# Optimization experiments

Measured on AMD Instinct MI355X. Metric: run time of the kernel, lower is better.

The kernel has to match this reference:

```python
import jax, jax.numpy as jnp
import numpy as np

B, W, H, C = 4, 32, 32, 128   # image feature map
S, D = 256, 512               # text seq len, text embed dim
NC = 64                       # num_channels (attention inner dim)


def setup_inputs() -> dict:
    key = jax.random.key(0)
    ks = jax.random.split(key, 16)
    def dense(k, din, dout):
        return jax.random.normal(k, (din, dout), jnp.float32) / np.sqrt(din)
    return {
        "x": jax.random.normal(ks[0], (B, W, H, C), jnp.float32),
        "s": jax.random.normal(ks[1], (B, S, D), jnp.float32),
        "a": jax.random.randint(ks[2], (B, S), 0, 2).astype(jnp.float32),
        "Wq": dense(ks[3], C, NC),  "bq": jnp.zeros((NC,), jnp.float32),
        "Wkx": dense(ks[4], C, NC), "bkx": jnp.zeros((NC,), jnp.float32),
        "Wvx": dense(ks[5], C, NC), "bvx": jnp.zeros((NC,), jnp.float32),
        "Wks": dense(ks[6], D, NC), "bks": jnp.zeros((NC,), jnp.float32),
        "Wvs": dense(ks[7], D, NC), "bvs": jnp.zeros((NC,), jnp.float32),
        "Wout": dense(ks[8], NC, C), "bout": jnp.zeros((C,), jnp.float32),
        "ln_scale": jnp.ones((C,), jnp.float32),
        "ln_bias": jnp.zeros((C,), jnp.float32),
    }


def reference(x, s, a, Wq, bq, Wkx, bkx, Wvx, bvx, Wks, bks, Wvs, bvs,
              Wout, bout, ln_scale, ln_bias):
    nc = Wq.shape[-1]
    # mask text embeddings: repeat(a,'b s -> b s d') * s
    te = s * a[:, :, None]
    # projections
    q = x @ Wq + bq            # (b,w,h,c)
    kx = x @ Wkx + bkx         # (b,w,h,c)
    vx = x @ Vx_dummy if False else x @ Wvx + bvx
    ks = te @ Wks + bks        # (b,s,c)
    vs = te @ Wvs + bvs        # (b,s,c)
    # broadcast-add spatial and text keys/values -> (b,w,h,s,c)
    k = kx[:, :, :, None, :] + ks[:, None, None, :, :]
    v = vx[:, :, :, None, :] + vs[:, None, None, :, :]
    # attention matrix over channels: v^T @ k contracted over s -> (b,w,h,c,c)
    attn = jnp.einsum('bwhsc,bwhsd->bwhcd', v, k) / jnp.sqrt(jnp.asarray(nc, x.dtype))
    attn = jax.nn.softmax(attn, axis=-1)
    # q applied through the channel-channel attention -> (b,w,h,c)
    out = jnp.einsum('bwhj,bwhjk->bwhk', q, attn)
    # output projection back to x channels, residual, layernorm
    out = out @ Wout + bout
    x = x + out
    mu = jnp.mean(x, axis=-1, keepdims=True)
    var = jnp.var(x, axis=-1, keepdims=True)
    x = (x - mu) * jax.lax.rsqrt(var + 1e-6) * ln_scale + ln_bias
    return x
```

## Files before the change

kernel.cpp:

```cpp
#include <hip/hip_runtime.h>
#include <hip/hip_bf16.h>

#define BB 4
#define SS 256
#define DD 512
#define CC 128
#define NC 64
#define PXB 8

__global__ __launch_bounds__(256) void text_proj_kernel(
    const float* __restrict__ s, const float* __restrict__ a,
    const float* __restrict__ Wks, const float* __restrict__ bks,
    const float* __restrict__ Wvs, const float* __restrict__ bvs,
    float* __restrict__ ksw, float* __restrict__ vsw)
{
    __shared__ float tel[4][DD];
    __shared__ float part[2][2][4][NC];
    const int t = threadIdx.x;
    const int w = t >> 6;
    const int lane = t & 63;
    const int row0 = blockIdx.x * 4;

    {
        const float4* s4 = (const float4*)(s + (size_t)row0 * DD);
        for (int i = t; i < 512; i += 256) {
            const int r = i >> 7;
            const float am = a[row0 + r];
            float4 v = s4[i];
            v.x *= am; v.y *= am; v.z *= am; v.w *= am;
            ((float4*)&tel[0][0])[i] = v;
        }
    }
    __syncthreads();

    const int m = w & 1;
    const int h = w >> 1;
    const float* __restrict__ Wm = m ? Wvs : Wks;
    const int kb = h * 256;
    float a0 = 0.f, a1 = 0.f, a2 = 0.f, a3 = 0.f;
    #pragma unroll 4
    for (int k = 0; k < 256; ++k) {
        const float wv = Wm[(size_t)(kb + k) * NC + lane];
        a0 = fmaf(tel[0][kb + k], wv, a0);
        a1 = fmaf(tel[1][kb + k], wv, a1);
        a2 = fmaf(tel[2][kb + k], wv, a2);
        a3 = fmaf(tel[3][kb + k], wv, a3);
    }
    part[m][h][0][lane] = a0; part[m][h][1][lane] = a1;
    part[m][h][2][lane] = a2; part[m][h][3][lane] = a3;
    __syncthreads();

    for (int i = t; i < 512; i += 256) {
        const int mm = i >> 8;
        const int r = (i >> 6) & 3;
        const int col = i & 63;
        const float v = part[mm][0][r][col] + part[mm][1][r][col]
                      + (mm ? bvs[col] : bks[col]);
        float* dst = mm ? vsw : ksw;
        dst[(size_t)(row0 + r) * NC + col] = v;
    }
}

__global__ __launch_bounds__(256) void reduce_kernel(
    const float* __restrict__ ksw, const float* __restrict__ vsw,
    float* __restrict__ Mw, float* __restrict__ Ksw, float* __restrict__ Vsw)
{
    __shared__ float pm[4][NC], pk[4][NC], pv[4];
    const int t = threadIdx.x, w = t >> 6, d = t & 63;
    const int b = blockIdx.x >> 6, c = blockIdx.x & 63;
    const float* __restrict__ vsb = vsw + (size_t)b * SS * NC;
    const float* __restrict__ ksb = ksw + (size_t)b * SS * NC;
    float acc = 0.f, ks_ = 0.f, vs_ = 0.f;
    #pragma unroll 4
    for (int j = 0; j < 64; ++j) {
        const int s2 = w * 64 + j;
        const float vv = vsb[s2 * NC + c];
        const float kv = ksb[s2 * NC + d];
        acc = fmaf(vv, kv, acc);
        ks_ += kv; vs_ += vv;
    }
    pm[w][d] = acc; pk[w][d] = ks_;
    if (d == 0) pv[w] = vs_;
    __syncthreads();
    if (t < 64) {
        Mw[((size_t)b * NC + c) * NC + t] = pm[0][t] + pm[1][t] + pm[2][t] + pm[3][t];
        if (c == 0) Ksw[b * NC + t] = pk[0][t] + pk[1][t] + pk[2][t] + pk[3][t];
        if (t == 0) Vsw[b * NC + c] = pv[0] + pv[1] + pv[2] + pv[3];
    }
}

__global__ __launch_bounds__(512) void pixel_kernel(
    const float* __restrict__ x,
    const float* __restrict__ Wq,  const float* __restrict__ bq,
    const float* __restrict__ Wkx, const float* __restrict__ bkx,
    const float* __restrict__ Wvx, const float* __restrict__ bvx,
    const float* __restrict__ Wout, const float* __restrict__ bout,
    const float* __restrict__ ln_scale, const float* __restrict__ ln_bias,
    const float* __restrict__ Mw, const float* __restrict__ Ksw,
    const float* __restrict__ Vsw,
    float* __restrict__ out)
{
    __shared__ float Wc[32 * 192];
    __shared__ float xl[PXB][CC];
    __shared__ float Ml[NC * 65];
    __shared__ float proj[3][PXB][NC];
    __shared__ float rsl[PXB][NC];
    __shared__ float mxl[PXB][NC];
    __shared__ float outl[PXB][NC];
    __shared__ float Ksl[NC], Vsl[NC];
    __shared__ float redl[4][2][4];

    const int t = threadIdx.x;
    const int w = t >> 6, lane = t & 63;
    const int px0g = blockIdx.x * PXB;
    const int b = px0g >> 10;

    {
        const float4* x4 = (const float4*)(x + (size_t)px0g * CC);
        for (int i = t; i < PXB * CC / 4; i += 512)
            ((float4*)&xl[0][0])[i] = x4[i];
        const float* Mb = Mw + (size_t)b * NC * NC;
        for (int i = t; i < NC * NC; i += 512)
            Ml[(i >> 6) * 65 + (i & 63)] = Mb[i];
        if (t < NC) { Ksl[t] = Ksw[b * NC + t]; Vsl[t] = Vsw[b * NC + t]; }
    }

    float4 pre0, pre1, pre2;
    {
        #pragma unroll
        for (int i = 0; i < 3; ++i) {
            const int flat = (t + i * 512) * 4;
            const int kk2 = flat / 192, col = flat % 192;
            const int seg = col >> 6, c0 = col & 63;
            const float* p = (seg == 0) ? Wq : (seg == 1 ? Wkx : Wvx);
            const float4 v = *(const float4*)(p + (size_t)kk2 * NC + c0);
            if (i == 0) pre0 = v; else if (i == 1) pre1 = v; else pre2 = v;
        }
    }
    const int mm = w % 3;
    const int g  = w / 3;
    float acc0 = 0.f, acc1 = 0.f, acc2 = 0.f, acc3 = 0.f;
    for (int kc = 0; kc < 4; ++kc) {
        ((float4*)Wc)[t]        = pre0;
        ((float4*)Wc)[t + 512]  = pre1;
        ((float4*)Wc)[t + 1024] = pre2;
        __syncthreads();
        if (kc < 3) {
            #pragma unroll
            for (int i = 0; i < 3; ++i) {
                const int flat = (t + i * 512) * 4;
                const int kk2 = flat / 192, col = flat % 192;
                const int seg = col >> 6, c0 = col & 63;
                const float* p = (seg == 0) ? Wq : (seg == 1 ? Wkx : Wvx);
                const float4 v = *(const float4*)(p + (size_t)((kc + 1) * 32 + kk2) * NC + c0);
                if (i == 0) pre0 = v; else if (i == 1) pre1 = v; else pre2 = v;
            }
        }
        if (w < 6) {
            const int kb = kc * 32;
            #pragma unroll
            for (int k4 = 0; k4 < 8; ++k4) {
                const float4 x0 = *(const float4*)&xl[4 * g + 0][kb + k4 * 4];
                const float4 x1 = *(const float4*)&xl[4 * g + 1][kb + k4 * 4];
                const float4 x2 = *(const float4*)&xl[4 * g + 2][kb + k4 * 4];
                const float4 x3 = *(const float4*)&xl[4 * g + 3][kb + k4 * 4];
                #pragma unroll
                for (int q = 0; q < 4; ++q) {
                    const float wv = Wc[(k4 * 4 + q) * 192 + mm * 64 + lane];
                    const float e0 = (q == 0) ? x0.x : (q == 1) ? x0.y : (q == 2) ? x0.z : x0.w;
                    const float e1 = (q == 0) ? x1.x : (q == 1) ? x1.y : (q == 2) ? x1.z : x1.w;
                    const float e2 = (q == 0) ? x2.x : (q == 1) ? x2.y : (q == 2) ? x2.z : x2.w;
                    const float e3 = (q == 0) ? x3.x : (q == 1) ? x3.y : (q == 2) ? x3.z : x3.w;
                    acc0 = fmaf(e0, wv, acc0);
                    acc1 = fmaf(e1, wv, acc1);
                    acc2 = fmaf(e2, wv, acc2);
                    acc3 = fmaf(e3, wv, acc3);
                }
            }
        }
        __syncthreads();
    }
    if (w < 6) {
        const float* bias = (mm == 0) ? bq : (mm == 1 ? bkx : bvx);
        const float bb = bias[lane];
        proj[mm][4 * g + 0][lane] = acc0 + bb;
        proj[mm][4 * g + 1][lane] = acc1 + bb;
        proj[mm][4 * g + 2][lane] = acc2 + bb;
        proj[mm][4 * g + 3][lane] = acc3 + bb;
    }
    __syncthreads();

    {
        const int px = w, c = lane;
        const float vxc = proj[2][px][c];
        const float qc  = proj[0][px][c];
        const float uc  = fmaf(256.0f, vxc, Vsl[c]);
        float row[NC];
        float mx = -3.4e38f;
        #pragma unroll
        for (int d = 0; d < NC; ++d) {
            const float A = fmaf(uc, proj[1][px][d],
                                 fmaf(vxc, Ksl[d], Ml[c * 65 + d])) * 0.125f;
            row[d] = A;
            mx = fmaxf(mx, A);
        }
        float sum = 0.f;
        #pragma unroll
        for (int d = 0; d < NC; ++d) sum += __expf(row[d] - mx);
        rsl[px][c] = qc / sum;
        mxl[px][c] = mx;
    }
    __syncthreads();

    {
        const int px = w, d = lane;
        const float kxd = proj[1][px][d];
        const float Ksd = Ksl[d];
        float acc = 0.f;
        #pragma unroll 4
        for (int c = 0; c < NC; ++c) {
            const float vxc = proj[2][px][c];
            const float uc = fmaf(256.0f, vxc, Vsl[c]);
            const float A = fmaf(uc, kxd, fmaf(vxc, Ksd, Ml[c * 65 + d])) * 0.125f;
            acc = fmaf(rsl[px][c], __expf(A - mxl[px][c]), acc);
        }
        outl[px][d] = acc;
    }
    __syncthreads();

    {
        const int col = t & 127;
        const int pxg = t >> 7;
        const int px0 = 2 * pxg, px1 = px0 + 1;
        float acc0 = 0.f, acc1 = 0.f;
        #pragma unroll 4
        for (int k = 0; k < NC; ++k) {
            const float wv = Wout[k * CC + col];
            acc0 = fmaf(outl[px0][k], wv, acc0);
            acc1 = fmaf(outl[px1][k], wv, acc1);
        }
        const float bb = bout[col];
        const float y0 = acc0 + bb + xl[px0][col];
        const float y1 = acc1 + bb + xl[px1][col];

        float s10 = y0, s20 = y0 * y0, s11 = y1, s21 = y1 * y1;
        #pragma unroll
        for (int off = 32; off >= 1; off >>= 1) {
            s10 += __shfl_down(s10, off);
            s20 += __shfl_down(s20, off);
            s11 += __shfl_down(s11, off);
            s21 += __shfl_down(s21, off);
        }
        const int half = (t >> 6) & 1;
        if (lane == 0) {
            redl[pxg][half][0] = s10; redl[pxg][half][1] = s20;
            redl[pxg][half][2] = s11; redl[pxg][half][3] = s21;
        }
        __syncthreads();
        const float S10 = redl[pxg][0][0] + redl[pxg][1][0];
        const float S20 = redl[pxg][0][1] + redl[pxg][1][1];
        const float S11 = redl[pxg][0][2] + redl[pxg][1][2];
        const float S21 = redl[pxg][0][3] + redl[pxg][1][3];
        const float mu0 = S10 * (1.f / 128.f);
        const float var0 = S20 * (1.f / 128.f) - mu0 * mu0;
        const float mu1 = S11 * (1.f / 128.f);
        const float var1 = S21 * (1.f / 128.f) - mu1 * mu1;
        const float r0 = rsqrtf(var0 + 1e-6f), r1 = rsqrtf(var1 + 1e-6f);
        const float gg = ln_scale[col], be = ln_bias[col];
        out[(size_t)(px0g + px0) * CC + col] = (y0 - mu0) * r0 * gg + be;
        out[(size_t)(px0g + px1) * CC + col] = (y1 - mu1) * r1 * gg + be;
    }
}

extern "C" void kernel_launch(void* const* d_in, const int* in_sizes, int n_in,
                              void* d_out, int out_size, void* d_ws, size_t ws_size,
                              hipStream_t stream) {
    const float* x        = (const float*)d_in[0];
    const float* s        = (const float*)d_in[1];
    const float* a        = (const float*)d_in[2];
    const float* Wq       = (const float*)d_in[3];
    const float* bq       = (const float*)d_in[4];
    const float* Wkx      = (const float*)d_in[5];
    const float* bkx      = (const float*)d_in[6];
    const float* Wvx      = (const float*)d_in[7];
    const float* bvx      = (const float*)d_in[8];
    const float* Wks      = (const float*)d_in[9];
    const float* bks      = (const float*)d_in[10];
    const float* Wvs      = (const float*)d_in[11];
    const float* bvs      = (const float*)d_in[12];
    const float* Wout     = (const float*)d_in[13];
    const float* bout     = (const float*)d_in[14];
    const float* ln_scale = (const float*)d_in[15];
    const float* ln_bias  = (const float*)d_in[16];

    float* ws  = (float*)d_ws;
    float* ksw = ws;
    float* vsw = ws + 65536;
    float* Mw  = ws + 131072;
    float* Ksw = ws + 147456;
    float* Vsw = ws + 147712;

    text_proj_kernel<<<(BB * SS) / 4, 256, 0, stream>>>(s, a, Wks, bks, Wvs, bvs, ksw, vsw);
    reduce_kernel<<<BB * NC, 256, 0, stream>>>(ksw, vsw, Mw, Ksw, Vsw);
    pixel_kernel<<<(BB * 1024) / PXB, 512, 0, stream>>>(
        x, Wq, bq, Wkx, bkx, Wvx, bvx, Wout, bout, ln_scale, ln_bias,
        Mw, Ksw, Vsw, (float*)d_out);
}
```

Before: 136.0 us.

## Split pixel projections into separate kernel and shrink per-block pixel tiles

Moves the q/kx/vx projections of x out of the pixel kernel into a standalone xproj kernel that writes a 192-wide projection buffer to workspace. The pixel kernel then loads these projections instead of staging weight chunks through shared memory, and drops to 4 pixels per block with 256 threads, doubling the block count. The text projection kernel is also reworked to handle 2 rows per block, with float4 weight loads and shuffle reductions across k-subgroups. This trades an extra launch and a global round-trip for the projections against higher occupancy and less synchronisation in the pixel kernel.

```diff
diff --git a/kernel.cpp b/kernel.cpp
--- a/kernel.cpp
+++ b/kernel.cpp
@@ -6,7 +6,49 @@
 #define DD 512
 #define CC 128
 #define NC 64
-#define PXB 8
+#define PXB 4
+
+__global__ __launch_bounds__(192) void xproj_kernel(
+    const float* __restrict__ x,
+    const float* __restrict__ Wq,  const float* __restrict__ bq,
+    const float* __restrict__ Wkx, const float* __restrict__ bkx,
+    const float* __restrict__ Wvx, const float* __restrict__ bvx,
+    float* __restrict__ P)
+{
+    __shared__ float xl[8][CC];
+    const int t = threadIdx.x;
+    const int w = t >> 6, lane = t & 63;
+    const int px0 = blockIdx.x * 8;
+
+    {
+        const float4* x4 = (const float4*)(x + (size_t)px0 * CC);
+        for (int i = t; i < 8 * CC / 4; i += 192)
+            ((float4*)&xl[0][0])[i] = x4[i];
+    }
+    __syncthreads();
+
+    const float* __restrict__ Wm = (w == 0) ? Wq : (w == 1 ? Wkx : Wvx);
+    const float* __restrict__ bm = (w == 0) ? bq : (w == 1 ? bkx : bvx);
+    float a0=0.f,a1=0.f,a2=0.f,a3=0.f,a4=0.f,a5=0.f,a6=0.f,a7=0.f;
+    #pragma unroll 4
+    for (int k = 0; k < CC; ++k) {
+        const float wv = Wm[(size_t)k * NC + lane];
+        a0 = fmaf(xl[0][k], wv, a0);
+        a1 = fmaf(xl[1][k], wv, a1);
+        a2 = fmaf(xl[2][k], wv, a2);
+        a3 = fmaf(xl[3][k], wv, a3);
+        a4 = fmaf(xl[4][k], wv, a4);
+        a5 = fmaf(xl[5][k], wv, a5);
+        a6 = fmaf(xl[6][k], wv, a6);
+        a7 = fmaf(xl[7][k], wv, a7);
+    }
+    const float bb = bm[lane];
+    float* dst = P + (size_t)px0 * 192 + w * 64 + lane;
+    dst[0*192] = a0 + bb; dst[1*192] = a1 + bb;
+    dst[2*192] = a2 + bb; dst[3*192] = a3 + bb;
+    dst[4*192] = a4 + bb; dst[5*192] = a5 + bb;
+    dst[6*192] = a6 + bb; dst[7*192] = a7 + bb;
+}
 
 __global__ __launch_bounds__(256) void text_proj_kernel(
     const float* __restrict__ s, const float* __restrict__ a,
@@ -14,46 +56,56 @@
     const float* __restrict__ Wvs, const float* __restrict__ bvs,
     float* __restrict__ ksw, float* __restrict__ vsw)
 {
-    __shared__ float tel[4][DD];
-    __shared__ float part[2][2][4][NC];
+    __shared__ float tel[2][DD];
+    __shared__ float part[2][2][2][NC];
     const int t = threadIdx.x;
-    const int w = t >> 6;
-    const int lane = t & 63;
-    const int row0 = blockIdx.x * 4;
+    const int w = t >> 6, lane = t & 63;
+    const int row0 = blockIdx.x * 2;
 
     {
         const float4* s4 = (const float4*)(s + (size_t)row0 * DD);
-        for (int i = t; i < 512; i += 256) {
-            const int r = i >> 7;
-            const float am = a[row0 + r];
-            float4 v = s4[i];
-            v.x *= am; v.y *= am; v.z *= am; v.w *= am;
-            ((float4*)&tel[0][0])[i] = v;
-        }
-    }
-    __syncthreads();
-
-    const int m = w & 1;
-    const int h = w >> 1;
+        const int i = t;
+        const int r = i >> 7;
+        const float am = a[row0 + r];
+        float4 v = s4[i];
+        v.x *= am; v.y *= am; v.z *= am; v.w *= am;
+        ((float4*)&tel[0][0])[i] = v;
+    }
+    __syncthreads();
+
+    const int m = w & 1, h = w >> 1;
+    const int kb = h * 256;
+    const int cg = (lane & 15) * 4;
+    const int ksub = lane >> 4;
     const float* __restrict__ Wm = m ? Wvs : Wks;
-    const int kb = h * 256;
-    float a0 = 0.f, a1 = 0.f, a2 = 0.f, a3 = 0.f;
+
+    float4 acc0 = {0,0,0,0}, acc1 = {0,0,0,0};
     #pragma unroll 4
-    for (int k = 0; k < 256; ++k) {
-        const float wv = Wm[(size_t)(kb + k) * NC + lane];
-        a0 = fmaf(tel[0][kb + k], wv, a0);
-        a1 = fmaf(tel[1][kb + k], wv, a1);
-        a2 = fmaf(tel[2][kb + k], wv, a2);
-        a3 = fmaf(tel[3][kb + k], wv, a3);
-    }
-    part[m][h][0][lane] = a0; part[m][h][1][lane] = a1;
-    part[m][h][2][lane] = a2; part[m][h][3][lane] = a3;
-    __syncthreads();
-
-    for (int i = t; i < 512; i += 256) {
-        const int mm = i >> 8;
-        const int r = (i >> 6) & 3;
-        const int col = i & 63;
+    for (int j = 0; j < 64; ++j) {
+        const int k = kb + 4 * j + ksub;
+        const float4 wv = *(const float4*)(Wm + (size_t)k * NC + cg);
+        const float t0 = tel[0][k];
+        const float t1 = tel[1][k];
+        acc0.x = fmaf(t0, wv.x, acc0.x); acc0.y = fmaf(t0, wv.y, acc0.y);
+        acc0.z = fmaf(t0, wv.z, acc0.z); acc0.w = fmaf(t0, wv.w, acc0.w);
+        acc1.x = fmaf(t1, wv.x, acc1.x); acc1.y = fmaf(t1, wv.y, acc1.y);
+        acc1.z = fmaf(t1, wv.z, acc1.z); acc1.w = fmaf(t1, wv.w, acc1.w);
+    }
+    #pragma unroll
+    for (int off = 16; off <= 32; off <<= 1) {
+        acc0.x += __shfl_down(acc0.x, off); acc0.y += __shfl_down(acc0.y, off);
+        acc0.z += __shfl_down(acc0.z, off); acc0.w += __shfl_down(acc0.w, off);
+        acc1.x += __shfl_down(acc1.x, off); acc1.y += __shfl_down(acc1.y, off);
+        acc1.z += __shfl_down(acc1.z, off); acc1.w += __shfl_down(acc1.w, off);
+    }
+    if (lane < 16) {
+        *(float4*)&part[m][h][0][cg] = acc0;
+        *(float4*)&part[m][h][1][cg] = acc1;
+    }
+    __syncthreads();
+
+    {
+        const int mm = t >> 7, r = (t >> 6) & 1, col = t & 63;
         const float v = part[mm][0][r][col] + part[mm][1][r][col]
                       + (mm ? bvs[col] : bks[col]);
         float* dst = mm ? vsw : ksw;
@@ -89,26 +141,22 @@
     }
 }
 
-__global__ __launch_bounds__(512) void pixel_kernel(
-    const float* __restrict__ x,
-    const float* __restrict__ Wq,  const float* __restrict__ bq,
-    const float* __restrict__ Wkx, const float* __restrict__ bkx,
-    const float* __restrict__ Wvx, const float* __restrict__ bvx,
+__global__ __launch_bounds__(256) void pixel_kernel(
+    const float* __restrict__ x, const float* __restrict__ P,
     const float* __restrict__ Wout, const float* __restrict__ bout,
     const float* __restrict__ ln_scale, const float* __restrict__ ln_bias,
     const float* __restrict__ Mw, const float* __restrict__ Ksw,
     const float* __restrict__ Vsw,
     float* __restrict__ out)
 {
-    __shared__ float Wc[32 * 192];
+    __shared__ float Ml[NC * 65];
+    __shared__ float projl[PXB][192];
     __shared__ float xl[PXB][CC];
-    __shared__ float Ml[NC * 65];
-    __shared__ float proj[3][PXB][NC];
     __shared__ float rsl[PXB][NC];
     __shared__ float mxl[PXB][NC];
     __shared__ float outl[PXB][NC];
     __shared__ float Ksl[NC], Vsl[NC];
-    __shared__ float redl[4][2][4];
+    __shared__ float redl[2][2][4];
 
     const int t = threadIdx.x;
     const int w = t >> 6, lane = t & 63;
@@ -116,90 +164,29 @@
     const int b = px0g >> 10;
 
     {
+        const float4* P4 = (const float4*)(P + (size_t)px0g * 192);
+        for (int i = t; i < PXB * 192 / 4; i += 256)
+            ((float4*)&projl[0][0])[i] = P4[i];
         const float4* x4 = (const float4*)(x + (size_t)px0g * CC);
-        for (int i = t; i < PXB * CC / 4; i += 512)
+        for (int i = t; i < PXB * CC / 4; i += 256)
             ((float4*)&xl[0][0])[i] = x4[i];
         const float* Mb = Mw + (size_t)b * NC * NC;
-        for (int i = t; i < NC * NC; i += 512)
+        for (int i = t; i < NC * NC; i += 256)
             Ml[(i >> 6) * 65 + (i & 63)] = Mb[i];
         if (t < NC) { Ksl[t] = Ksw[b * NC + t]; Vsl[t] = Vsw[b * NC + t]; }
     }
-
-    float4 pre0, pre1, pre2;
-    {
-        #pragma unroll
-        for (int i = 0; i < 3; ++i) {
-            const int flat = (t + i * 512) * 4;
-            const int kk2 = flat / 192, col = flat % 192;
-            const int seg = col >> 6, c0 = col & 63;
-            const float* p = (seg == 0) ? Wq : (seg == 1 ? Wkx : Wvx);
-            const float4 v = *(const float4*)(p + (size_t)kk2 * NC + c0);
-            if (i == 0) pre0 = v; else if (i == 1) pre1 = v; else pre2 = v;
-        }
-    }
-    const int mm = w % 3;
-    const int g  = w / 3;
-    float acc0 = 0.f, acc1 = 0.f, acc2 = 0.f, acc3 = 0.f;
-    for (int kc = 0; kc < 4; ++kc) {
-        ((float4*)Wc)[t]        = pre0;
-        ((float4*)Wc)[t + 512]  = pre1;
-        ((float4*)Wc)[t + 1024] = pre2;
-        __syncthreads();
-        if (kc < 3) {
-            #pragma unroll
-            for (int i = 0; i < 3; ++i) {
-                const int flat = (t + i * 512) * 4;
-                const int kk2 = flat / 192, col = flat % 192;
-                const int seg = col >> 6, c0 = col & 63;
-                const float* p = (seg == 0) ? Wq : (seg == 1 ? Wkx : Wvx);
-                const float4 v = *(const float4*)(p + (size_t)((kc + 1) * 32 + kk2) * NC + c0);
-                if (i == 0) pre0 = v; else if (i == 1) pre1 = v; else pre2 = v;
-            }
-        }
-        if (w < 6) {
-            const int kb = kc * 32;
-            #pragma unroll
-            for (int k4 = 0; k4 < 8; ++k4) {
-                const float4 x0 = *(const float4*)&xl[4 * g + 0][kb + k4 * 4];
-                const float4 x1 = *(const float4*)&xl[4 * g + 1][kb + k4 * 4];
-                const float4 x2 = *(const float4*)&xl[4 * g + 2][kb + k4 * 4];
-                const float4 x3 = *(const float4*)&xl[4 * g + 3][kb + k4 * 4];
-                #pragma unroll
-                for (int q = 0; q < 4; ++q) {
-                    const float wv = Wc[(k4 * 4 + q) * 192 + mm * 64 + lane];
-                    const float e0 = (q == 0) ? x0.x : (q == 1) ? x0.y : (q == 2) ? x0.z : x0.w;
-                    const float e1 = (q == 0) ? x1.x : (q == 1) ? x1.y : (q == 2) ? x1.z : x1.w;
-                    const float e2 = (q == 0) ? x2.x : (q == 1) ? x2.y : (q == 2) ? x2.z : x2.w;
-                    const float e3 = (q == 0) ? x3.x : (q == 1) ? x3.y : (q == 2) ? x3.z : x3.w;
-                    acc0 = fmaf(e0, wv, acc0);
-                    acc1 = fmaf(e1, wv, acc1);
-                    acc2 = fmaf(e2, wv, acc2);
-                    acc3 = fmaf(e3, wv, acc3);
-                }
-            }
-        }
-        __syncthreads();
-    }
-    if (w < 6) {
-        const float* bias = (mm == 0) ? bq : (mm == 1 ? bkx : bvx);
-        const float bb = bias[lane];
-        proj[mm][4 * g + 0][lane] = acc0 + bb;
-        proj[mm][4 * g + 1][lane] = acc1 + bb;
-        proj[mm][4 * g + 2][lane] = acc2 + bb;
-        proj[mm][4 * g + 3][lane] = acc3 + bb;
-    }
     __syncthreads();
 
     {
         const int px = w, c = lane;
-        const float vxc = proj[2][px][c];
-        const float qc  = proj[0][px][c];
+        const float vxc = projl[px][128 + c];
+        const float qc  = projl[px][c];
         const float uc  = fmaf(256.0f, vxc, Vsl[c]);
         float row[NC];
         float mx = -3.4e38f;
         #pragma unroll
         for (int d = 0; d < NC; ++d) {
-            const float A = fmaf(uc, proj[1][px][d],
+            const float A = fmaf(uc, projl[px][64 + d],
                                  fmaf(vxc, Ksl[d], Ml[c * 65 + d])) * 0.125f;
             row[d] = A;
             mx = fmaxf(mx, A);
@@ -214,12 +201,12 @@
 
     {
         const int px = w, d = lane;
-        const float kxd = proj[1][px][d];
+        const float kxd = projl[px][64 + d];
         const float Ksd = Ksl[d];
         float acc = 0.f;
         #pragma unroll 4
         for (int c = 0; c < NC; ++c) {
-            const float vxc = proj[2][px][c];
+            const float vxc = projl[px][128 + c];
             const float uc = fmaf(256.0f, vxc, Vsl[c]);
             const float A = fmaf(uc, kxd, fmaf(vxc, Ksd, Ml[c * 65 + d])) * 0.125f;
             acc = fmaf(rsl[px][c], __expf(A - mxl[px][c]), acc);
@@ -299,10 +286,11 @@
     float* Mw  = ws + 131072;
     float* Ksw = ws + 147456;
     float* Vsw = ws + 147712;
-
-    text_proj_kernel<<<(BB * SS) / 4, 256, 0, stream>>>(s, a, Wks, bks, Wvs, bvs, ksw, vsw);
+    float* Pw  = ws + 147968;
+
+    xproj_kernel<<<512, 192, 0, stream>>>(x, Wq, bq, Wkx, bkx, Wvx, bvx, Pw);
+    text_proj_kernel<<<(BB * SS) / 2, 256, 0, stream>>>(s, a, Wks, bks, Wvs, bvs, ksw, vsw);
     reduce_kernel<<<BB * NC, 256, 0, stream>>>(ksw, vsw, Mw, Ksw, Vsw);
-    pixel_kernel<<<(BB * 1024) / PXB, 512, 0, stream>>>(
-        x, Wq, bq, Wkx, bkx, Wvx, bvx, Wout, bout, ln_scale, ln_bias,
-        Mw, Ksw, Vsw, (float*)d_out);
-}
+    pixel_kernel<<<(BB * 1024) / PXB, 256, 0, stream>>>(
+        x, Pw, Wout, bout, ln_scale, ln_bias, Mw, Ksw, Vsw, (float*)d_out);
+}
```

Measured after the change: 127.6 us. -6.2%, faster.
